# Optimization experiments

Hardware: AMD Instinct MI355X
Metric: run time of the kernel (lower is better)

## Reference

```python
import jax, jax.numpy as jnp
import numpy as np

E, T, D, H = 8, 2048, 1024, 4096
N_LAYER = 12

def setup_inputs() -> dict:
    key = jax.random.key(0)
    ks = jax.random.split(key, 4)
    x = jax.random.normal(ks[0], (E, T, D), dtype=jnp.float32)
    w_c_fc = jax.random.normal(ks[1], (E, D, H), dtype=jnp.float32) * 0.02
    w_gate = jax.random.normal(ks[2], (E, D, H), dtype=jnp.float32) * 0.02
    w_c_proj = jax.random.normal(ks[3], (E, H, D), dtype=jnp.float32) * (0.02 * (2 * N_LAYER) ** (-0.5))
    b_c_fc = jnp.zeros((E, 1, H), dtype=jnp.float32)
    b_gate = jnp.zeros((E, 1, H), dtype=jnp.float32)
    b_c_proj = jnp.zeros((E, 1, D), dtype=jnp.float32)
    return {"x": x, "w_c_fc": w_c_fc, "b_c_fc": b_c_fc, "w_gate": w_gate,
            "b_gate": b_gate, "w_c_proj": w_c_proj, "b_c_proj": b_c_proj}

def reference(x, w_c_fc, b_c_fc, w_gate, b_gate, w_c_proj, b_c_proj):
    # Per-expert SwiGLU FFN (grouped GEMM over expert dim e)
    h = jnp.einsum('eti,eih->eth', x, w_c_fc) + b_c_fc      # [E,T,H]
    g = jax.nn.silu(jnp.einsum('eti,eih->eth', x, w_gate) + b_gate)
    og = h * g                                               # gated hidden
    o = jnp.einsum('eth,eho->eto', og, w_c_proj) + b_c_proj  # [E,T,D]
    return o
```

## Files before the change

### kernel.cpp

```cpp
#include <hip/hip_runtime.h>

#define E 8
#define T 2048
#define D 1024
#define H 4096

using f32x4 = __attribute__((ext_vector_type(4))) float;
using frag8 = __attribute__((ext_vector_type(8))) short;

typedef unsigned int uint_as3 __attribute__((address_space(3)));
typedef unsigned int uint_as1 __attribute__((address_space(1)));

__device__ __forceinline__ unsigned short f2bf(float f) {
  unsigned int u = __float_as_uint(f);
  u += 0x7fffu + ((u >> 16) & 1u);
  return (unsigned short)(u >> 16);
}

__device__ __forceinline__ void gload16(const void* g, void* l) {
  __builtin_amdgcn_global_load_lds((const uint_as1*)g, (uint_as3*)l, 16, 0, 0);
}

__device__ __forceinline__ void stage8(const unsigned short* src, int ld,
                                       unsigned short* lds, int r0, int lane) {
  int lr = lane >> 3;
  int cs = lane & 7;
  int gc = cs ^ lr;
  const unsigned short* g = src + (size_t)(r0 + lr) * ld + gc * 8;
  unsigned short* l = lds + r0 * 64;
  gload16(g, l);
}

__device__ __forceinline__ frag8 read_frag(const unsigned short* lds, int row, int chunk) {
  return *(const frag8*)&lds[row * 64 + ((chunk ^ (row & 7)) << 3)];
}

#define BARRIER() asm volatile("s_barrier" ::: "memory")
#define WAIT_LGKM0() asm volatile("s_waitcnt lgkmcnt(0)" ::: "memory")


__global__ __launch_bounds__(256) void convert_kernel(const float4* __restrict__ in,
                                                      ushort4* __restrict__ out, int n4) {
  int i = blockIdx.x * blockDim.x + threadIdx.x;
  int stride = gridDim.x * blockDim.x;
  for (; i < n4; i += stride) {
    float4 v = in[i];
    ushort4 o;
    o.x = f2bf(v.x); o.y = f2bf(v.y); o.z = f2bf(v.z); o.w = f2bf(v.w);
    out[i] = o;
  }
}

__global__ __launch_bounds__(256) void tconv_kernel(const float* __restrict__ in,
                                                    unsigned short* __restrict__ out,
                                                    int R, int C) {
  __shared__ float tile[32][33];
  int e = blockIdx.z;
  const float* src = in + (size_t)e * R * C;
  unsigned short* dst = out + (size_t)e * R * C;
  int c0 = blockIdx.x * 32, r0 = blockIdx.y * 32;
  int tx = threadIdx.x, ty = threadIdx.y;
#pragma unroll
  for (int i = 0; i < 32; i += 8)
    tile[ty + i][tx] = src[(size_t)(r0 + ty + i) * C + c0 + tx];
  __syncthreads();
#pragma unroll
  for (int i = 0; i < 32; i += 8)
    dst[(size_t)(c0 + ty + i) * R + r0 + tx] = f2bf(tile[tx][ty + i]);
}


__global__ __launch_bounds__(512) void gemm1_kernel(
    const unsigned short* __restrict__ xb,
    const unsigned short* __restrict__ wfcT,
    const unsigned short* __restrict__ wgT,
    const float* __restrict__ bfc,
    const float* __restrict__ bgate,
    unsigned short* __restrict__ og) {
  __shared__ unsigned short As[3][128 * 64];
  __shared__ unsigned short Bf[3][128 * 64];
  __shared__ unsigned short Bg[3][128 * 64];

  int bid = blockIdx.x;
  int e = bid >> 9;
  int mt = (bid >> 5) & 15;
  int nt = bid & 31;
  int m0 = mt * 128, n0 = nt * 128;

  int tid = threadIdx.x;
  int w = __builtin_amdgcn_readfirstlane(tid >> 6);
  int lane = tid & 63;

  const unsigned short* Ab = xb + (size_t)e * T * D + (size_t)m0 * D;
  const unsigned short* Fb = wfcT + (size_t)e * H * D + (size_t)n0 * D;
  const unsigned short* Gb = wgT + (size_t)e * H * D + (size_t)n0 * D;

  f32x4 ah[4][2] = {};
  f32x4 ag[4][2] = {};

  int wm = (w >> 2) * 64;
  int wn = (w & 3) * 32;
  int col = lane & 15, quad = lane >> 4;
  int r0a = w * 8;

  constexpr int NT = D / 64;

#pragma unroll
  for (int t0 = 0; t0 < 2; ++t0) {
    stage8(Ab + t0 * 64, D, As[t0], r0a, lane);
    stage8(Ab + t0 * 64, D, As[t0], r0a + 64, lane);
    stage8(Fb + t0 * 64, D, Bf[t0], r0a, lane);
    stage8(Fb + t0 * 64, D, Bf[t0], r0a + 64, lane);
    stage8(Gb + t0 * 64, D, Bg[t0], r0a, lane);
    stage8(Gb + t0 * 64, D, Bg[t0], r0a + 64, lane);
  }
  asm volatile("s_waitcnt vmcnt(6)" ::: "memory");
  BARRIER();

  int s = 0, s2 = 2;
  for (int t = 0; t < NT; ++t) {
    const unsigned short* Asl = As[s];
    const unsigned short* Bfl = Bf[s];
    const unsigned short* Bgl = Bg[s];
    bool pf = (t + 2) < NT;
    int kpre = (t + 2) * 64;

    frag8 a[4], f[2], g[2];
#pragma unroll
    for (int i = 0; i < 4; ++i) a[i] = read_frag(Asl, wm + i * 16 + col, quad);
#pragma unroll
    for (int i = 0; i < 2; ++i) {
      f[i] = read_frag(Bfl, wn + i * 16 + col, quad);
      g[i] = read_frag(Bgl, wn + i * 16 + col, quad);
    }
    if (pf) {
      stage8(Ab + kpre, D, As[s2], r0a, lane);
      stage8(Ab + kpre, D, As[s2], r0a + 64, lane);
      stage8(Fb + kpre, D, Bf[s2], r0a, lane);
    }
    BARRIER();
    WAIT_LGKM0();
    __builtin_amdgcn_sched_barrier(0);
    __builtin_amdgcn_s_setprio(1);
#pragma unroll
    for (int mi = 0; mi < 4; ++mi)
#pragma unroll
      for (int ni = 0; ni < 2; ++ni) {
        ah[mi][ni] = __builtin_amdgcn_mfma_f32_16x16x32_bf16(a[mi], f[ni], ah[mi][ni], 0, 0, 0);
        ag[mi][ni] = __builtin_amdgcn_mfma_f32_16x16x32_bf16(a[mi], g[ni], ag[mi][ni], 0, 0, 0);
      }
    __builtin_amdgcn_s_setprio(0);
    BARRIER();

#pragma unroll
    for (int i = 0; i < 4; ++i) a[i] = read_frag(Asl, wm + i * 16 + col, 4 + quad);
#pragma unroll
    for (int i = 0; i < 2; ++i) {
      f[i] = read_frag(Bfl, wn + i * 16 + col, 4 + quad);
      g[i] = read_frag(Bgl, wn + i * 16 + col, 4 + quad);
    }
    if (pf) {
      stage8(Fb + kpre, D, Bf[s2], r0a + 64, lane);
      stage8(Gb + kpre, D, Bg[s2], r0a, lane);
      stage8(Gb + kpre, D, Bg[s2], r0a + 64, lane);
    }
    BARRIER();
    WAIT_LGKM0();
    __builtin_amdgcn_sched_barrier(0);
    __builtin_amdgcn_s_setprio(1);
#pragma unroll
    for (int mi = 0; mi < 4; ++mi)
#pragma unroll
      for (int ni = 0; ni < 2; ++ni) {
        ah[mi][ni] = __builtin_amdgcn_mfma_f32_16x16x32_bf16(a[mi], f[ni], ah[mi][ni], 0, 0, 0);
        ag[mi][ni] = __builtin_amdgcn_mfma_f32_16x16x32_bf16(a[mi], g[ni], ag[mi][ni], 0, 0, 0);
      }
    __builtin_amdgcn_s_setprio(0);
    if (pf)
      asm volatile("s_waitcnt vmcnt(6)" ::: "memory");
    else if (t + 2 == NT)
      asm volatile("s_waitcnt vmcnt(0)" ::: "memory");
    BARRIER();

    s = (s == 2) ? 0 : s + 1;
    s2 = (s2 == 2) ? 0 : s2 + 1;
  }

#pragma unroll
  for (int ni = 0; ni < 2; ++ni) {
    int n = n0 + wn + ni * 16 + col;
    float bh = bfc[e * H + n];
    float bg2 = bgate[e * H + n];
#pragma unroll
    for (int mi = 0; mi < 4; ++mi) {
#pragma unroll
      for (int i = 0; i < 4; ++i) {
        int m = m0 + wm + mi * 16 + quad * 4 + i;
        float hv = ah[mi][ni][i] + bh;
        float gv = ag[mi][ni][i] + bg2;
        float sg = gv / (1.0f + __expf(-gv));
        og[(size_t)e * T * H + (size_t)m * H + n] = f2bf(hv * sg);
      }
    }
  }
}


__global__ __launch_bounds__(512) void gemm2_kernel(
    const unsigned short* __restrict__ og,
    const unsigned short* __restrict__ wpT,
    const float* __restrict__ bproj,
    float* __restrict__ out) {
  __shared__ unsigned short As[3][256 * 64];
  __shared__ unsigned short Bs[3][128 * 64];

  int bid = blockIdx.x;
  int e = bid >> 6;
  int mt = (bid >> 3) & 7;
  int nt = bid & 7;
  int m0 = mt * 256, n0 = nt * 128;

  int tid = threadIdx.x;
  int w = __builtin_amdgcn_readfirstlane(tid >> 6);
  int lane = tid & 63;

  const unsigned short* Ab = og + (size_t)e * T * H + (size_t)m0 * H;
  const unsigned short* Bb = wpT + (size_t)e * D * H + (size_t)n0 * H;

  f32x4 acc[4][4] = {};

  int wm = (w >> 1) * 64;
  int wn = (w & 1) * 64;
  int col = lane & 15, quad = lane >> 4;
  int r0a = w * 8;

  constexpr int NT = H / 64;

#pragma unroll
  for (int t0 = 0; t0 < 2; ++t0) {
    stage8(Ab + t0 * 64, H, As[t0], r0a, lane);
    stage8(Ab + t0 * 64, H, As[t0], r0a + 64, lane);
    stage8(Ab + t0 * 64, H, As[t0], r0a + 128, lane);
    stage8(Ab + t0 * 64, H, As[t0], r0a + 192, lane);
    stage8(Bb + t0 * 64, H, Bs[t0], r0a, lane);
    stage8(Bb + t0 * 64, H, Bs[t0], r0a + 64, lane);
  }
  asm volatile("s_waitcnt vmcnt(6)" ::: "memory");
  BARRIER();

  int s = 0, s2 = 2;
  for (int t = 0; t < NT; ++t) {
    const unsigned short* Asl = As[s];
    const unsigned short* Bsl = Bs[s];
    bool pf = (t + 2) < NT;
    int kpre = (t + 2) * 64;

    frag8 a[4], b[4];
#pragma unroll
    for (int i = 0; i < 4; ++i) a[i] = read_frag(Asl, wm + i * 16 + col, quad);
#pragma unroll
    for (int i = 0; i < 4; ++i) b[i] = read_frag(Bsl, wn + i * 16 + col, quad);
    if (pf) {
      stage8(Ab + kpre, H, As[s2], r0a, lane);
      stage8(Ab + kpre, H, As[s2], r0a + 64, lane);
      stage8(Bb + kpre, H, Bs[s2], r0a, lane);
    }
    BARRIER();
    WAIT_LGKM0();
    __builtin_amdgcn_sched_barrier(0);
    __builtin_amdgcn_s_setprio(1);
#pragma unroll
    for (int mi = 0; mi < 4; ++mi)
#pragma unroll
      for (int ni = 0; ni < 4; ++ni)
        acc[mi][ni] = __builtin_amdgcn_mfma_f32_16x16x32_bf16(a[mi], b[ni], acc[mi][ni], 0, 0, 0);
    __builtin_amdgcn_s_setprio(0);
    BARRIER();

#pragma unroll
    for (int i = 0; i < 4; ++i) a[i] = read_frag(Asl, wm + i * 16 + col, 4 + quad);
#pragma unroll
    for (int i = 0; i < 4; ++i) b[i] = read_frag(Bsl, wn + i * 16 + col, 4 + quad);
    if (pf) {
      stage8(Ab + kpre, H, As[s2], r0a + 128, lane);
      stage8(Ab + kpre, H, As[s2], r0a + 192, lane);
      stage8(Bb + kpre, H, Bs[s2], r0a + 64, lane);
    }
    BARRIER();
    WAIT_LGKM0();
    __builtin_amdgcn_sched_barrier(0);
    __builtin_amdgcn_s_setprio(1);
#pragma unroll
    for (int mi = 0; mi < 4; ++mi)
#pragma unroll
      for (int ni = 0; ni < 4; ++ni)
        acc[mi][ni] = __builtin_amdgcn_mfma_f32_16x16x32_bf16(a[mi], b[ni], acc[mi][ni], 0, 0, 0);
    __builtin_amdgcn_s_setprio(0);
    if (pf)
      asm volatile("s_waitcnt vmcnt(6)" ::: "memory");
    else if (t + 2 == NT)
      asm volatile("s_waitcnt vmcnt(0)" ::: "memory");
    BARRIER();

    s = (s == 2) ? 0 : s + 1;
    s2 = (s2 == 2) ? 0 : s2 + 1;
  }

#pragma unroll
  for (int ni = 0; ni < 4; ++ni) {
    int n = n0 + wn + ni * 16 + col;
    float bb = bproj[e * D + n];
#pragma unroll
    for (int mi = 0; mi < 4; ++mi) {
#pragma unroll
      for (int i = 0; i < 4; ++i) {
        int m = m0 + wm + mi * 16 + quad * 4 + i;
        out[(size_t)e * T * D + (size_t)m * D + n] = acc[mi][ni][i] + bb;
      }
    }
  }
}


extern "C" void kernel_launch(void* const* d_in, const int* in_sizes, int n_in,
                              void* d_out, int out_size, void* d_ws, size_t ws_size,
                              hipStream_t stream) {
  const float* x = (const float*)d_in[0];
  const float* wfc = (const float*)d_in[1];
  const float* bfc = (const float*)d_in[2];
  const float* wg = (const float*)d_in[3];
  const float* bg = (const float*)d_in[4];
  const float* wp = (const float*)d_in[5];
  const float* bp = (const float*)d_in[6];
  float* out = (float*)d_out;

  char* ws = (char*)d_ws;
  unsigned short* xb = (unsigned short*)(ws);
  unsigned short* wfcT = (unsigned short*)(ws + 33554432);
  unsigned short* wgT = (unsigned short*)(ws + 100663296);
  unsigned short* wpT = (unsigned short*)(ws + 167772160);
  unsigned short* og = (unsigned short*)(ws + 234881024);

  convert_kernel<<<2048, 256, 0, stream>>>((const float4*)x, (ushort4*)xb,
                                           (int)((size_t)E * T * D / 4));
  tconv_kernel<<<dim3(H / 32, D / 32, E), dim3(32, 8), 0, stream>>>(wfc, wfcT, D, H);
  tconv_kernel<<<dim3(H / 32, D / 32, E), dim3(32, 8), 0, stream>>>(wg, wgT, D, H);
  tconv_kernel<<<dim3(D / 32, H / 32, E), dim3(32, 8), 0, stream>>>(wp, wpT, H, D);

  gemm1_kernel<<<E * (T / 128) * (H / 128), 512, 0, stream>>>(xb, wfcT, wgT, bfc, bg, og);
  gemm2_kernel<<<E * (T / 256) * (D / 128), 512, 0, stream>>>(og, wpT, bp, out);
}
```

Before: 1.010 ms.

## Merge split K-half phases into one per-iteration phase and reorder gemm2 blocks

In both GEMM kernels, each 64-wide K tile used to be processed in two half-phases, each with its own barriers and lgkmcnt waits. Now all LDS fragments for both halves are read up front, all prefetches for the tile are issued together, and the MFMAs run back to back, leaving one barrier per iteration. This cuts barrier and wait overhead and gives the compiler freedom to interleave the LDS reads with the MFMAs. It costs more live fragment registers, which could lower occupancy, and it drops the explicit sched_barrier and waitcnt, leaving their placement to the compiler. Separately, gemm2 now maps block IDs expert-fastest, changing which tiles run concurrently and how they share cache.

```diff
diff --git a/kernel.cpp b/kernel.cpp
--- a/kernel.cpp
+++ b/kernel.cpp
@@ -36,7 +36,6 @@
 }
 
 #define BARRIER() asm volatile("s_barrier" ::: "memory")
-#define WAIT_LGKM0() asm volatile("s_waitcnt lgkmcnt(0)" ::: "memory")
 
 
 __global__ __launch_bounds__(256) void convert_kernel(const float4* __restrict__ in,
@@ -125,57 +124,44 @@
     bool pf = (t + 2) < NT;
     int kpre = (t + 2) * 64;
 
-    frag8 a[4], f[2], g[2];
-#pragma unroll
-    for (int i = 0; i < 4; ++i) a[i] = read_frag(Asl, wm + i * 16 + col, quad);
+    frag8 a0[4], f0[2], g0[2], a1[4], f1[2], g1[2];
+#pragma unroll
+    for (int i = 0; i < 4; ++i) {
+      a0[i] = read_frag(Asl, wm + i * 16 + col, quad);
+      a1[i] = read_frag(Asl, wm + i * 16 + col, 4 + quad);
+    }
 #pragma unroll
     for (int i = 0; i < 2; ++i) {
-      f[i] = read_frag(Bfl, wn + i * 16 + col, quad);
-      g[i] = read_frag(Bgl, wn + i * 16 + col, quad);
+      f0[i] = read_frag(Bfl, wn + i * 16 + col, quad);
+      f1[i] = read_frag(Bfl, wn + i * 16 + col, 4 + quad);
+      g0[i] = read_frag(Bgl, wn + i * 16 + col, quad);
+      g1[i] = read_frag(Bgl, wn + i * 16 + col, 4 + quad);
     }
     if (pf) {
       stage8(Ab + kpre, D, As[s2], r0a, lane);
       stage8(Ab + kpre, D, As[s2], r0a + 64, lane);
       stage8(Fb + kpre, D, Bf[s2], r0a, lane);
-    }
-    BARRIER();
-    WAIT_LGKM0();
-    __builtin_amdgcn_sched_barrier(0);
-    __builtin_amdgcn_s_setprio(1);
-#pragma unroll
-    for (int mi = 0; mi < 4; ++mi)
-#pragma unroll
-      for (int ni = 0; ni < 2; ++ni) {
-        ah[mi][ni] = __builtin_amdgcn_mfma_f32_16x16x32_bf16(a[mi], f[ni], ah[mi][ni], 0, 0, 0);
-        ag[mi][ni] = __builtin_amdgcn_mfma_f32_16x16x32_bf16(a[mi], g[ni], ag[mi][ni], 0, 0, 0);
-      }
-    __builtin_amdgcn_s_setprio(0);
-    BARRIER();
-
-#pragma unroll
-    for (int i = 0; i < 4; ++i) a[i] = read_frag(Asl, wm + i * 16 + col, 4 + quad);
-#pragma unroll
-    for (int i = 0; i < 2; ++i) {
-      f[i] = read_frag(Bfl, wn + i * 16 + col, 4 + quad);
-      g[i] = read_frag(Bgl, wn + i * 16 + col, 4 + quad);
-    }
-    if (pf) {
       stage8(Fb + kpre, D, Bf[s2], r0a + 64, lane);
       stage8(Gb + kpre, D, Bg[s2], r0a, lane);
       stage8(Gb + kpre, D, Bg[s2], r0a + 64, lane);
     }
-    BARRIER();
-    WAIT_LGKM0();
-    __builtin_amdgcn_sched_barrier(0);
     __builtin_amdgcn_s_setprio(1);
 #pragma unroll
     for (int mi = 0; mi < 4; ++mi)
 #pragma unroll
       for (int ni = 0; ni < 2; ++ni) {
-        ah[mi][ni] = __builtin_amdgcn_mfma_f32_16x16x32_bf16(a[mi], f[ni], ah[mi][ni], 0, 0, 0);
-        ag[mi][ni] = __builtin_amdgcn_mfma_f32_16x16x32_bf16(a[mi], g[ni], ag[mi][ni], 0, 0, 0);
+        ah[mi][ni] = __builtin_amdgcn_mfma_f32_16x16x32_bf16(a0[mi], f0[ni], ah[mi][ni], 0, 0, 0);
+        ag[mi][ni] = __builtin_amdgcn_mfma_f32_16x16x32_bf16(a0[mi], g0[ni], ag[mi][ni], 0, 0, 0);
+      }
+#pragma unroll
+    for (int mi = 0; mi < 4; ++mi)
+#pragma unroll
+      for (int ni = 0; ni < 2; ++ni) {
+        ah[mi][ni] = __builtin_amdgcn_mfma_f32_16x16x32_bf16(a1[mi], f1[ni], ah[mi][ni], 0, 0, 0);
+        ag[mi][ni] = __builtin_amdgcn_mfma_f32_16x16x32_bf16(a1[mi], g1[ni], ag[mi][ni], 0, 0, 0);
       }
     __builtin_amdgcn_s_setprio(0);
+
     if (pf)
       asm volatile("s_waitcnt vmcnt(6)" ::: "memory");
     else if (t + 2 == NT)
@@ -215,9 +201,10 @@
   __shared__ unsigned short Bs[3][128 * 64];
 
   int bid = blockIdx.x;
-  int e = bid >> 6;
-  int mt = (bid >> 3) & 7;
-  int nt = bid & 7;
+  int e = bid & 7;
+  int idx = bid >> 3;
+  int mt = idx >> 3;
+  int nt = idx & 7;
   int m0 = mt * 256, n0 = nt * 128;
 
   int tid = threadIdx.x;
@@ -255,47 +242,35 @@
     bool pf = (t + 2) < NT;
     int kpre = (t + 2) * 64;
 
-    frag8 a[4], b[4];
-#pragma unroll
-    for (int i = 0; i < 4; ++i) a[i] = read_frag(Asl, wm + i * 16 + col, quad);
-#pragma unroll
-    for (int i = 0; i < 4; ++i) b[i] = read_frag(Bsl, wn + i * 16 + col, quad);
+    frag8 a0[4], b0[4], a1[4], b1[4];
+#pragma unroll
+    for (int i = 0; i < 4; ++i) {
+      a0[i] = read_frag(Asl, wm + i * 16 + col, quad);
+      a1[i] = read_frag(Asl, wm + i * 16 + col, 4 + quad);
+      b0[i] = read_frag(Bsl, wn + i * 16 + col, quad);
+      b1[i] = read_frag(Bsl, wn + i * 16 + col, 4 + quad);
+    }
     if (pf) {
       stage8(Ab + kpre, H, As[s2], r0a, lane);
       stage8(Ab + kpre, H, As[s2], r0a + 64, lane);
-      stage8(Bb + kpre, H, Bs[s2], r0a, lane);
-    }
-    BARRIER();
-    WAIT_LGKM0();
-    __builtin_amdgcn_sched_barrier(0);
-    __builtin_amdgcn_s_setprio(1);
-#pragma unroll
-    for (int mi = 0; mi < 4; ++mi)
-#pragma unroll
-      for (int ni = 0; ni < 4; ++ni)
-        acc[mi][ni] = __builtin_amdgcn_mfma_f32_16x16x32_bf16(a[mi], b[ni], acc[mi][ni], 0, 0, 0);
-    __builtin_amdgcn_s_setprio(0);
-    BARRIER();
-
-#pragma unroll
-    for (int i = 0; i < 4; ++i) a[i] = read_frag(Asl, wm + i * 16 + col, 4 + quad);
-#pragma unroll
-    for (int i = 0; i < 4; ++i) b[i] = read_frag(Bsl, wn + i * 16 + col, 4 + quad);
-    if (pf) {
       stage8(Ab + kpre, H, As[s2], r0a + 128, lane);
       stage8(Ab + kpre, H, As[s2], r0a + 192, lane);
+      stage8(Bb + kpre, H, Bs[s2], r0a, lane);
       stage8(Bb + kpre, H, Bs[s2], r0a + 64, lane);
     }
-    BARRIER();
-    WAIT_LGKM0();
-    __builtin_amdgcn_sched_barrier(0);
     __builtin_amdgcn_s_setprio(1);
 #pragma unroll
     for (int mi = 0; mi < 4; ++mi)
 #pragma unroll
       for (int ni = 0; ni < 4; ++ni)
-        acc[mi][ni] = __builtin_amdgcn_mfma_f32_16x16x32_bf16(a[mi], b[ni], acc[mi][ni], 0, 0, 0);
+        acc[mi][ni] = __builtin_amdgcn_mfma_f32_16x16x32_bf16(a0[mi], b0[ni], acc[mi][ni], 0, 0, 0);
+#pragma unroll
+    for (int mi = 0; mi < 4; ++mi)
+#pragma unroll
+      for (int ni = 0; ni < 4; ++ni)
+        acc[mi][ni] = __builtin_amdgcn_mfma_f32_16x16x32_bf16(a1[mi], b1[ni], acc[mi][ni], 0, 0, 0);
     __builtin_amdgcn_s_setprio(0);
+
     if (pf)
       asm volatile("s_waitcnt vmcnt(6)" ::: "memory");
     else if (t + 2 == NT)
```

Result: faster. 883.7 us (-12.5%).
